# Kernel tuning notes

Measured on AMD Instinct MI355X. Metric: run time of the kernel, lower is better.

The kernel has to match this reference:

```python
import jax, jax.numpy as jnp
import numpy as np

B, N, DIM, H = 8, 1024, 512, 8
D = DIM // H
SCALE = DIM ** -0.5


def setup_inputs() -> dict:
    key = jax.random.key(0)
    ks = jax.random.split(key, 8)
    s = 0.02
    return {
        "x": jax.random.normal(ks[0], (B, N, DIM), dtype=jnp.float32),
        "mask": jax.random.uniform(ks[1], (1, 1, N, N), dtype=jnp.float32),
        "Wqkv1": jax.random.normal(ks[2], (DIM, 3 * DIM), dtype=jnp.float32) * s,
        "bqkv1": jnp.zeros((3 * DIM,), dtype=jnp.float32),
        "Wqkv2": jax.random.normal(ks[3], (DIM, 3 * DIM), dtype=jnp.float32) * s,
        "bqkv2": jnp.zeros((3 * DIM,), dtype=jnp.float32),
        "Wnn1": jax.random.normal(ks[4], (DIM, DIM), dtype=jnp.float32) * s,
        "bnn1": jnp.zeros((DIM,), dtype=jnp.float32),
    }


def _split_heads(qkv, b, n):
    # qkv: [b, n, 3*dim] -> three [b, h, n, d]
    q, k, v = jnp.split(qkv, 3, axis=-1)
    r = lambda t: t.reshape(b, n, H, D).transpose(0, 2, 1, 3)
    return r(q), r(k), r(v)


def reference(x, mask, Wqkv1, bqkv1, Wqkv2, bqkv2, Wnn1, bnn1):
    b, n, dim = x.shape
    # Stage 1: mask-scaled sigmoid attention (no softmax, no scale)
    q, k, v = _split_heads(x @ Wqkv1 + bqkv1, b, n)
    dots = jax.nn.sigmoid(jnp.einsum('bhid,bhjd->bhij', q, k) * mask)
    out1 = jnp.einsum('bhij,bhjd->bhid', dots, v)
    out1 = out1.transpose(0, 2, 1, 3).reshape(b, n, dim)
    # Stage 2: standard scaled softmax attention on stage-1 output
    q, k, v = _split_heads(out1 @ Wqkv2 + bqkv2, b, n)
    attn = jax.nn.softmax(jnp.einsum('bhid,bhjd->bhij', q, k) * SCALE, axis=-1)
    out = jnp.einsum('bhij,bhjd->bhid', attn, v)
    out = out.transpose(0, 2, 1, 3).reshape(b, n, dim)
    # Output projection (dropout is identity in eval mode)
    return out @ Wnn1 + bnn1
```

## Files before the change

### kernel.cpp

```cpp
#include <hip/hip_runtime.h>
#include <hip/hip_bf16.h>
#include <stdint.h>

constexpr int B_ = 8, N_ = 1024, DIM_ = 512, H_ = 8, D_ = 64;
constexpr int BH_ = B_ * H_;
constexpr int M_  = B_ * N_;
constexpr float SCALE_ = 0.04419417382415922f;
constexpr float LOG2E_ = 1.44269504088896f;
constexpr float QSL2E_ = SCALE_ * LOG2E_;

typedef __bf16 bf16x8 __attribute__((ext_vector_type(8)));
typedef float  f32x4  __attribute__((ext_vector_type(4)));
typedef unsigned short u16;
typedef u16 u16x8 __attribute__((ext_vector_type(8)));
typedef u16 u16x4 __attribute__((ext_vector_type(4)));

static __device__ __forceinline__ u16 f2bf(float f) {
  uint32_t u = __builtin_bit_cast(uint32_t, f);
  u += 0x7FFFu + ((u >> 16) & 1u);
  return (u16)(u >> 16);
}
static __device__ __forceinline__ bf16x8 ld8(const u16* p) {
  return __builtin_bit_cast(bf16x8, *reinterpret_cast<const u16x8*>(p));
}
static __device__ __forceinline__ f32x4 mfma16(bf16x8 a, bf16x8 b, f32x4 c) {
  return __builtin_amdgcn_mfma_f32_16x16x32_bf16(a, b, c, 0, 0, 0);
}
static __device__ __forceinline__ void gload_lds16(const u16* g, void* l) {
  __builtin_amdgcn_global_load_lds(
      (const __attribute__((address_space(1))) void*)g,
      (__attribute__((address_space(3))) void*)l, 16, 0, 0);
}

__global__ void k_cvt(const float* __restrict__ in, u16* __restrict__ out, int n4) {
  int i = blockIdx.x * blockDim.x + threadIdx.x;
  int stride = gridDim.x * blockDim.x;
  for (int idx = i; idx < n4; idx += stride) {
    float4 v = reinterpret_cast<const float4*>(in)[idx];
    u16x4 o;
    o[0] = f2bf(v.x); o[1] = f2bf(v.y); o[2] = f2bf(v.z); o[3] = f2bf(v.w);
    reinterpret_cast<u16x4*>(out)[idx] = o;
  }
}

__global__ void k_mask(const float* __restrict__ in, float* __restrict__ out, int n4) {
  int i = blockIdx.x * blockDim.x + threadIdx.x;
  int stride = gridDim.x * blockDim.x;
  for (int idx = i; idx < n4; idx += stride) {
    float4 v = reinterpret_cast<const float4*>(in)[idx];
    v.x *= -LOG2E_; v.y *= -LOG2E_; v.z *= -LOG2E_; v.w *= -LOG2E_;
    reinterpret_cast<float4*>(out)[idx] = v;
  }
}

__global__ void k_wt(const float* __restrict__ W, u16* __restrict__ Wt, int ncols, float qs) {
  int idx = blockIdx.x * 256 + threadIdx.x;
  if (idx >= ncols * 512) return;
  int c = idx >> 9, k = idx & 511;
  float v = W[k * ncols + c];
  if (c < 512) v *= qs;
  Wt[idx] = f2bf(v);
}

template<int NC, int MODE, bool SQ>
__global__ __launch_bounds__(256) void k_gemm(
    const u16* __restrict__ A, const u16* __restrict__ Wt, const float* __restrict__ bias,
    u16* __restrict__ qo, u16* __restrict__ ko, u16* __restrict__ vto, float* __restrict__ fo)
{
  __shared__ __attribute__((aligned(16))) u16 As[2][128 * 32];
  __shared__ __attribute__((aligned(16))) u16 Bs[2][128 * 32];
  const int wv = threadIdx.x >> 6, ln = threadIdx.x & 63;
  const int lr = ln & 15, lg = ln >> 4;
  const int wr = wv >> 1, wc = wv & 1;
  const int r0 = blockIdx.x * 128;
  const int c0 = blockIdx.y * 128;

  auto stage = [&](int bufi, int kk) {
#pragma unroll
    for (int q = 0; q < 2; ++q) {
      int L = (wv * 2 + q) * 1024 + ln * 16;
      int row = L >> 6;
      int col = ((L & 63) ^ (((row >> 1) & 3) << 4)) >> 1;
      gload_lds16(A  + (size_t)(r0 + row) * 512 + kk + col, (char*)As[bufi] + (wv * 2 + q) * 1024);
      gload_lds16(Wt + (size_t)(c0 + row) * 512 + kk + col, (char*)Bs[bufi] + (wv * 2 + q) * 1024);
    }
  };
  auto swzld = [&](const u16* tile, int row, int colb) -> bf16x8 {
    int byte = (row << 6) + (colb ^ (((row >> 1) & 3) << 4));
    return __builtin_bit_cast(bf16x8, *reinterpret_cast<const u16x8*>((const char*)tile + byte));
  };

  f32x4 acc[4][4] = {};
  stage(0, 0);
  int buf = 0;
  for (int kk = 0; kk < 512; kk += 32) {
    __syncthreads();
    if (kk + 32 < 512) stage(buf ^ 1, kk + 32);
    bf16x8 af[4], bfb[4];
#pragma unroll
    for (int m = 0; m < 4; ++m) af[m]  = swzld(As[buf], wr * 64 + m * 16 + lr, lg * 16);
#pragma unroll
    for (int n = 0; n < 4; ++n) bfb[n] = swzld(Bs[buf], wc * 64 + n * 16 + lr, lg * 16);
#pragma unroll
    for (int m = 0; m < 4; ++m)
#pragma unroll
      for (int n = 0; n < 4; ++n)
        acc[m][n] = mfma16(af[m], bfb[n], acc[m][n]);
    buf ^= 1;
  }

#pragma unroll
  for (int m = 0; m < 4; ++m)
#pragma unroll
    for (int n = 0; n < 4; ++n)
#pragma unroll
      for (int r = 0; r < 4; ++r) {
        int gr = r0 + wr * 64 + m * 16 + lg * 4 + r;
        int gc = c0 + wc * 64 + n * 16 + lr;
        float bsc = (SQ && gc < 512) ? QSL2E_ : 1.f;
        float v = acc[m][n][r] + bias[gc] * bsc;
        if (MODE == 0) {
          int part = gc >> 9, cc = gc & 511;
          int hh = cc >> 6, dd = cc & 63;
          int bb = gr >> 10, nn = gr & 1023;
          int bh = bb * H_ + hh;
          u16 bv = f2bf(v);
          if (part == 0)      qo[((size_t)(bh * N_ + nn)) * D_ + dd] = bv;
          else if (part == 1) ko[((size_t)(bh * N_ + nn)) * D_ + dd] = bv;
          else                vto[((size_t)(bh * D_ + dd)) * N_ + nn] = bv;
        } else {
          fo[(size_t)gr * NC + gc] = v;
        }
      }
}

template<int STAGE>
__global__ __launch_bounds__(512, 4) void k_attn(
    const u16* __restrict__ Q, const u16* __restrict__ K, const u16* __restrict__ Vt,
    const float* __restrict__ mask, u16* __restrict__ O)
{
  __shared__ __attribute__((aligned(16))) u16 Kb[2][64 * 64];
  __shared__ __attribute__((aligned(16))) u16 Vb[2][64 * 64];
  __shared__ __attribute__((aligned(16))) u16 pbuf[8][16][72];
  const int wv = threadIdx.x >> 6, ln = threadIdx.x & 63;
  const int lr = ln & 15, lg = ln >> 4;
  const int bh = blockIdx.y;
  const int i0 = blockIdx.x * 128 + wv * 16;
  const size_t base = (size_t)bh * N_ * D_;

  auto stageKV = [&](int bufi, int jt2) {
    int L = wv * 1024 + ln * 16;
    int row = L >> 7;
    int col = ((L & 127) ^ ((row & 7) << 4)) >> 1;
    gload_lds16(K  + base + (size_t)(jt2 + row) * 64 + col,  (char*)Kb[bufi] + wv * 1024);
    gload_lds16(Vt + base + (size_t)row * 1024 + jt2 + col,  (char*)Vb[bufi] + wv * 1024);
  };
  auto swzld = [&](const u16* tile, int row, int colb) -> bf16x8 {
    int byte = (row << 7) + (colb ^ ((row & 7) << 4));
    return __builtin_bit_cast(bf16x8, *reinterpret_cast<const u16x8*>((const char*)tile + byte));
  };

  bf16x8 aq0 = ld8(Q + base + (size_t)(i0 + lr) * D_ + lg * 8);
  bf16x8 aq1 = ld8(Q + base + (size_t)(i0 + lr) * D_ + 32 + lg * 8);

  f32x4 acco[4] = {};
  float ssum_ln = 0.f;

  stageKV(0, 0);
  int buf = 0;
  for (int jt = 0; jt < N_; jt += 64) {
    __syncthreads();
    if (jt + 64 < N_) stageKV(buf ^ 1, jt + 64);

    f32x4 s[4];
    __builtin_amdgcn_s_setprio(1);
#pragma unroll
    for (int js = 0; js < 4; ++js) {
      int krow = js * 16 + lr;
      bf16x8 bk0 = swzld(Kb[buf], krow, lg * 16);
      bf16x8 bk1 = swzld(Kb[buf], krow, 64 + lg * 16);
      f32x4 z = {};
      z = mfma16(bk0, aq0, z);
      z = mfma16(bk1, aq1, z);
      s[js] = z;
    }
    __builtin_amdgcn_s_setprio(0);

    if (STAGE == 1) {
#pragma unroll
      for (int js = 0; js < 4; ++js) {
        const float4 mk = *reinterpret_cast<const float4*>(
            &mask[(size_t)(i0 + lr) * N_ + jt + js * 16 + lg * 4]);
        u16x4 w;
#pragma unroll
        for (int r = 0; r < 4; ++r) {
          float mkr = (r == 0) ? mk.x : (r == 1) ? mk.y : (r == 2) ? mk.z : mk.w;
          float e = exp2f(s[js][r] * mkr);
          float p = __builtin_amdgcn_rcpf(1.f + e);
          w[r] = f2bf(p);
        }
        *reinterpret_cast<u16x4*>(&pbuf[wv][lr][js * 16 + lg * 4]) = w;
      }
    } else {
      float ps = 0.f;
#pragma unroll
      for (int js = 0; js < 4; ++js) {
        u16x4 w;
#pragma unroll
        for (int r = 0; r < 4; ++r) {
          float p = exp2f(s[js][r]);
          ps += p;
          w[r] = f2bf(p);
        }
        *reinterpret_cast<u16x4*>(&pbuf[wv][lr][js * 16 + lg * 4]) = w;
      }
      ssum_ln += ps;
    }

    bf16x8 ap0 = ld8(&pbuf[wv][lr][lg * 8]);
    bf16x8 ap1 = ld8(&pbuf[wv][lr][32 + lg * 8]);
    __builtin_amdgcn_s_setprio(1);
#pragma unroll
    for (int db = 0; db < 4; ++db) {
      bf16x8 bv0 = swzld(Vb[buf], db * 16 + lr, lg * 16);
      bf16x8 bv1 = swzld(Vb[buf], db * 16 + lr, 64 + lg * 16);
      acco[db] = mfma16(ap1, bv1, mfma16(ap0, bv0, acco[db]));
    }
    __builtin_amdgcn_s_setprio(0);
    buf ^= 1;
  }

  float inv[4];
  if (STAGE == 2) {
    float st = ssum_ln;
    st += __shfl_xor(st, 16);
    st += __shfl_xor(st, 32);
#pragma unroll
    for (int r = 0; r < 4; ++r)
      inv[r] = __builtin_amdgcn_rcpf(__shfl(st, lg * 4 + r));
  }

  const int bb = bh >> 3, hh = bh & 7;
#pragma unroll
  for (int db = 0; db < 4; ++db)
#pragma unroll
    for (int r = 0; r < 4; ++r) {
      float v = acco[db][r];
      if (STAGE == 2) v *= inv[r];
      int gi = i0 + lg * 4 + r;
      O[(size_t)(bb * N_ + gi) * DIM_ + hh * D_ + db * 16 + lr] = f2bf(v);
    }
}

extern "C" void kernel_launch(void* const* d_in, const int* in_sizes, int n_in,
                              void* d_out, int out_size, void* d_ws, size_t ws_size,
                              hipStream_t stream)
{
  const float* x    = (const float*)d_in[0];
  const float* mask = (const float*)d_in[1];
  const float* W1   = (const float*)d_in[2];
  const float* b1   = (const float*)d_in[3];
  const float* W2   = (const float*)d_in[4];
  const float* b2   = (const float*)d_in[5];
  const float* W3   = (const float*)d_in[6];
  const float* b3   = (const float*)d_in[7];
  float* out = (float*)d_out;

  char* ws = (char*)d_ws;
  size_t off = 0;
  auto alloc = [&](size_t bytes) { char* p = ws + off; off += (bytes + 255) & ~255ULL; return p; };
  u16*   W1t = (u16*)alloc((size_t)1536 * 512 * 2);
  u16*   W2t = (u16*)alloc((size_t)1536 * 512 * 2);
  u16*   W3t = (u16*)alloc((size_t)512 * 512 * 2);
  u16*   xb  = (u16*)alloc((size_t)M_ * DIM_ * 2);
  u16*   q   = (u16*)alloc((size_t)BH_ * N_ * D_ * 2);
  u16*   k   = (u16*)alloc((size_t)BH_ * N_ * D_ * 2);
  u16*   vt  = (u16*)alloc((size_t)BH_ * N_ * D_ * 2);
  u16*   o1  = (u16*)alloc((size_t)M_ * DIM_ * 2);
  float* mk  = (float*)alloc((size_t)N_ * N_ * 4);
  u16*   o2  = xb;

  k_cvt<<<2048, 256, 0, stream>>>(x, xb, M_ * DIM_ / 4);
  k_mask<<<1024, 256, 0, stream>>>(mask, mk, N_ * N_ / 4);
  k_wt<<<(1536 * 512 + 255) / 256, 256, 0, stream>>>(W1, W1t, 1536, 1.f);
  k_wt<<<(1536 * 512 + 255) / 256, 256, 0, stream>>>(W2, W2t, 1536, QSL2E_);
  k_wt<<<(512 * 512 + 255) / 256, 256, 0, stream>>>(W3, W3t, 512, 1.f);

  dim3 g1(M_ / 128, 1536 / 128);
  k_gemm<1536, 0, false><<<g1, 256, 0, stream>>>(xb, W1t, b1, q, k, vt, nullptr);

  dim3 ga(N_ / 128, BH_);
  k_attn<1><<<ga, 512, 0, stream>>>(q, k, vt, mk, o1);

  k_gemm<1536, 0, true><<<g1, 256, 0, stream>>>(o1, W2t, b2, q, k, vt, nullptr);

  k_attn<2><<<ga, 512, 0, stream>>>(q, k, vt, mk, o2);

  dim3 g3(M_ / 128, 512 / 128);
  k_gemm<512, 1, false><<<g3, 256, 0, stream>>>(o2, W3t, b3, nullptr, nullptr, nullptr, out);
}
```

Before: 252.5 us.

## Vectorize epilogue stores, prefetch mask a tile ahead, use native bf16 convert

```diff
diff --git a/kernel.cpp b/kernel.cpp
--- a/kernel.cpp
+++ b/kernel.cpp
@@ -16,9 +16,7 @@
 typedef u16 u16x4 __attribute__((ext_vector_type(4)));
 
 static __device__ __forceinline__ u16 f2bf(float f) {
-  uint32_t u = __builtin_bit_cast(uint32_t, f);
-  u += 0x7FFFu + ((u >> 16) & 1u);
-  return (u16)(u >> 16);
+  return __builtin_bit_cast(u16, (__bf16)f);
 }
 static __device__ __forceinline__ bf16x8 ld8(const u16* p) {
   return __builtin_bit_cast(bf16x8, *reinterpret_cast<const u16x8*>(p));
@@ -112,26 +110,32 @@
 #pragma unroll
   for (int m = 0; m < 4; ++m)
 #pragma unroll
-    for (int n = 0; n < 4; ++n)
-#pragma unroll
-      for (int r = 0; r < 4; ++r) {
-        int gr = r0 + wr * 64 + m * 16 + lg * 4 + r;
-        int gc = c0 + wc * 64 + n * 16 + lr;
-        float bsc = (SQ && gc < 512) ? QSL2E_ : 1.f;
-        float v = acc[m][n][r] + bias[gc] * bsc;
-        if (MODE == 0) {
-          int part = gc >> 9, cc = gc & 511;
-          int hh = cc >> 6, dd = cc & 63;
-          int bb = gr >> 10, nn = gr & 1023;
-          int bh = bb * H_ + hh;
-          u16 bv = f2bf(v);
-          if (part == 0)      qo[((size_t)(bh * N_ + nn)) * D_ + dd] = bv;
-          else if (part == 1) ko[((size_t)(bh * N_ + nn)) * D_ + dd] = bv;
-          else                vto[((size_t)(bh * D_ + dd)) * N_ + nn] = bv;
+    for (int n = 0; n < 4; ++n) {
+      const int gc  = c0 + wc * 64 + n * 16 + lr;
+      const int gr0 = r0 + wr * 64 + m * 16 + lg * 4;
+      const float bsc = (SQ && gc < 512) ? QSL2E_ : 1.f;
+      const float bv = bias[gc] * bsc;
+      if (MODE == 0) {
+        const int part = gc >> 9, cc = gc & 511;
+        const int hh = cc >> 6, dd = cc & 63;
+        const int bb = gr0 >> 10, nn = gr0 & 1023;
+        const int bh = bb * H_ + hh;
+        if (part == 2) {
+          u16x4 w;
+#pragma unroll
+          for (int r = 0; r < 4; ++r) w[r] = f2bf(acc[m][n][r] + bv);
+          *reinterpret_cast<u16x4*>(&vto[((size_t)(bh * D_ + dd)) * N_ + nn]) = w;
         } else {
-          fo[(size_t)gr * NC + gc] = v;
+          u16* dst = (part == 0 ? qo : ko) + ((size_t)(bh * N_ + nn)) * D_ + dd;
+#pragma unroll
+          for (int r = 0; r < 4; ++r) dst[(size_t)r * D_] = f2bf(acc[m][n][r] + bv);
         }
+      } else {
+#pragma unroll
+        for (int r = 0; r < 4; ++r)
+          fo[(size_t)(gr0 + r) * NC + gc] = acc[m][n][r] + bv;
       }
+    }
 }
 
 template<int STAGE>
@@ -166,6 +170,15 @@
   f32x4 acco[4] = {};
   float ssum_ln = 0.f;
 
+  float4 mk[4];
+  const float* mrow = mask + (size_t)(i0 + lr) * N_;
+  auto loadmask = [&](int jt2) {
+#pragma unroll
+    for (int js = 0; js < 4; ++js)
+      mk[js] = *reinterpret_cast<const float4*>(&mrow[jt2 + js * 16 + lg * 4]);
+  };
+  if (STAGE == 1) loadmask(0);
+
   stageKV(0, 0);
   int buf = 0;
   for (int jt = 0; jt < N_; jt += 64) {
@@ -189,18 +202,16 @@
     if (STAGE == 1) {
 #pragma unroll
       for (int js = 0; js < 4; ++js) {
-        const float4 mk = *reinterpret_cast<const float4*>(
-            &mask[(size_t)(i0 + lr) * N_ + jt + js * 16 + lg * 4]);
         u16x4 w;
 #pragma unroll
         for (int r = 0; r < 4; ++r) {
-          float mkr = (r == 0) ? mk.x : (r == 1) ? mk.y : (r == 2) ? mk.z : mk.w;
+          float mkr = (r == 0) ? mk[js].x : (r == 1) ? mk[js].y : (r == 2) ? mk[js].z : mk[js].w;
           float e = exp2f(s[js][r] * mkr);
-          float p = __builtin_amdgcn_rcpf(1.f + e);
-          w[r] = f2bf(p);
+          w[r] = f2bf(__builtin_amdgcn_rcpf(1.f + e));
         }
         *reinterpret_cast<u16x4*>(&pbuf[wv][lr][js * 16 + lg * 4]) = w;
       }
+      if (jt + 64 < N_) loadmask(jt + 64);
     } else {
       float ps = 0.f;
 #pragma unroll
@@ -240,16 +251,20 @@
       inv[r] = __builtin_amdgcn_rcpf(__shfl(st, lg * 4 + r));
   }
 
-  const int bb = bh >> 3, hh = bh & 7;
 #pragma unroll
   for (int db = 0; db < 4; ++db)
 #pragma unroll
     for (int r = 0; r < 4; ++r) {
       float v = acco[db][r];
       if (STAGE == 2) v *= inv[r];
-      int gi = i0 + lg * 4 + r;
-      O[(size_t)(bb * N_ + gi) * DIM_ + hh * D_ + db * 16 + lr] = f2bf(v);
-    }
+      pbuf[wv][lg * 4 + r][db * 16 + lr] = f2bf(v);
+    }
+  bf16x8 o0v = ld8(&pbuf[wv][lr][lg * 8]);
+  bf16x8 o1v = ld8(&pbuf[wv][lr][32 + lg * 8]);
+  const int bb = bh >> 3, hh = bh & 7;
+  u16* orow = O + (size_t)(bb * N_ + i0 + lr) * DIM_ + hh * D_;
+  *reinterpret_cast<u16x8*>(orow + lg * 8)      = __builtin_bit_cast(u16x8, o0v);
+  *reinterpret_cast<u16x8*>(orow + 32 + lg * 8) = __builtin_bit_cast(u16x8, o1v);
 }
 
 extern "C" void kernel_launch(void* const* d_in, const int* in_sizes, int n_in,
```

New measurement: 228.5 us. 9.5% less time.
